# Performance work log

Measured on AMD Instinct MI355X. Metric: run time of the kernel, lower is better.

## Reference

```python
import math
import jax, jax.numpy as jnp
import numpy as np

B, S, D = 4, 2048, 512
H = 8
HD = D // H  # 64


def setup_inputs() -> dict:
    key = jax.random.key(0)
    k1, k2, k3, k4, k5 = jax.random.split(key, 5)
    x = jax.random.normal(k1, (B, S, D), dtype=jnp.float32)
    # additive causal mask, broadcast over [H, B, S, S] in the original code
    neg_inf = jnp.float32(-1e9)
    mask = jnp.where(jnp.tril(jnp.ones((S, S), dtype=bool)), 0.0, neg_inf).astype(jnp.float32)
    Wqkv = jax.random.normal(k2, (D, 3 * D), dtype=jnp.float32) * (1.0 / math.sqrt(D))
    bqkv = jax.random.normal(k3, (3 * D,), dtype=jnp.float32) * 0.02
    Wo = jax.random.normal(k4, (D, D), dtype=jnp.float32) * (1.0 / math.sqrt(D))
    bo = jax.random.normal(k5, (D,), dtype=jnp.float32) * 0.02
    return {"x": x, "mask": mask, "Wqkv": Wqkv, "bqkv": bqkv, "Wo": Wo, "bo": bo}


def reference(x, mask, Wqkv, bqkv, Wo, bo):
    b, s, d = x.shape
    hd = d // H
    qkv = x @ Wqkv + bqkv                       # [b, s, 3d]
    # match torch: reshape to [b, s, H, 3*hd], move heads, chunk last dim
    qkv = qkv.reshape(b, s, H, 3 * hd).transpose(0, 2, 1, 3)  # [b, H, s, 3hd]
    q, k, v = jnp.split(qkv, 3, axis=-1)        # each [b, H, s, hd]
    scale = 1.0 / math.sqrt(hd)
    scores = jnp.einsum('bhqd,bhkd->bhqk', q, k) * scale
    scores = scores + mask                      # mask [s, s] broadcasts over [b, H, s, s]
    attn = jax.nn.softmax(scores, axis=-1)
    vals = jnp.einsum('bhqk,bhkd->bhqd', attn, v)
    vals = vals.transpose(0, 2, 1, 3).reshape(b, s, d)
    return vals @ Wo + bo
```

## Files before the change

### kernel.cpp

```cpp
#include <hip/hip_runtime.h>
#include <hip/hip_bf16.h>

#define S_ 2048
#define D_ 512
#define HD_ 64
#define HH_ 8
#define M_ 8192

typedef __attribute__((ext_vector_type(8))) short short8;
typedef __attribute__((ext_vector_type(4))) short short4v;
typedef __attribute__((ext_vector_type(4))) float f32x4;

__device__ __forceinline__ unsigned short f2bf(float f) {
  unsigned u = __builtin_bit_cast(unsigned, f);
  u += 0x7fffu + ((u >> 16) & 1u);
  return (unsigned short)(u >> 16);
}

__device__ __forceinline__ f32x4 mfma16(short8 a, short8 b, f32x4 c) {
  return __builtin_amdgcn_mfma_f32_16x16x32_bf16(a, b, c, 0, 0, 0);
}

#define GLOAD_LDS16(gp, lp)                                                        \
  __builtin_amdgcn_global_load_lds(                                                \
      (const __attribute__((address_space(1))) void*)(gp),                         \
      (__attribute__((address_space(3))) void*)(lp), 16, 0, 0)

__global__ __launch_bounds__(256) void k_cvt_all(const float* __restrict__ x,
                                                 short* __restrict__ xb,
                                                 const float* __restrict__ wqkv,
                                                 short* __restrict__ wqkvt,
                                                 const float* __restrict__ wo,
                                                 short* __restrict__ wot) {
  __shared__ short T[32][33];
  const int bid = blockIdx.x;
  if (bid < 2048) {
    int idx = bid * 256 + threadIdx.x;
    const float4* p = (const float4*)x;
    float4 a = p[idx * 2];
    float4 b = p[idx * 2 + 1];
    short8 v;
    v[0] = (short)f2bf(a.x); v[1] = (short)f2bf(a.y);
    v[2] = (short)f2bf(a.z); v[3] = (short)f2bf(a.w);
    v[4] = (short)f2bf(b.x); v[5] = (short)f2bf(b.y);
    v[6] = (short)f2bf(b.z); v[7] = (short)f2bf(b.w);
    int row = idx >> 6;
    int dst = row * 512 + ((idx >> 3) & 7) * 64 + (((idx & 7) ^ (row & 7)) << 3);
    *(short8*)&xb[dst] = v;
    return;
  }
  const float* w;
  short* wt;
  int C, bx, by;
  if (bid < 2816) {
    w = wqkv; wt = wqkvt; C = 1536;
    int b = bid - 2048; bx = b % 48; by = b / 48;
  } else {
    w = wo; wt = wot; C = 512;
    int b = bid - 2816; bx = b % 16; by = b / 16;
  }
  const int tx = threadIdx.x & 31, ty = threadIdx.x >> 5;
  const int n0 = bx * 32, k0 = by * 32;
#pragma unroll
  for (int i = 0; i < 4; i++) {
    int k = k0 + ty + 8 * i;
    T[ty + 8 * i][tx] = (short)f2bf(w[k * C + n0 + tx]);
  }
  __syncthreads();
#pragma unroll
  for (int i = 0; i < 4; i++) {
    int n = n0 + ty + 8 * i;
    int k = k0 + tx;
    int ksw = (k & ~63) | ((((k >> 3) & 7) ^ (n & 7)) << 3) | (k & 7);
    wt[n * 512 + ksw] = T[tx][ty + 8 * i];
  }
}

template <int MODE>
__global__ __launch_bounds__(256) void k_gemm(const short* __restrict__ A,
                                              const short* __restrict__ Bt,
                                              const float* __restrict__ bias,
                                              short* __restrict__ Qo,
                                              short* __restrict__ Ko,
                                              short* __restrict__ VTo,
                                              float* __restrict__ Fo) {
  __shared__ short As[2][8192];
  __shared__ short Bs[2][4096];
  const int tid = threadIdx.x;
  const int w = tid >> 6, l = tid & 63, g = l >> 4, c = l & 15;
  const int lid = blockIdx.x;
  const int lidp = (lid & 7) * 192 + (lid >> 3);
  const int bm = (lidp / 24) * 128, bn = (lidp % 24) * 64;
  const int wm = (w >> 1) * 64, wn = (w & 1) * 32;
  f32x4 acc[4][2] = {};
  const short* Ap = A + (bm + (l >> 3)) * 512 + (l & 7) * 8;
  const short* Bp = Bt + (bn + (l >> 3)) * 512 + (l & 7) * 8;
  const int sa0 = w * 4;
  const int sb0 = w * 2;

#define GSTAGE(buf, k0)                                                       \
  {                                                                           \
    GLOAD_LDS16(Ap + (sa0 + 0) * 4096 + (k0), &As[buf][(sa0 + 0) * 512]);     \
    GLOAD_LDS16(Ap + (sa0 + 1) * 4096 + (k0), &As[buf][(sa0 + 1) * 512]);     \
    GLOAD_LDS16(Ap + (sa0 + 2) * 4096 + (k0), &As[buf][(sa0 + 2) * 512]);     \
    GLOAD_LDS16(Ap + (sa0 + 3) * 4096 + (k0), &As[buf][(sa0 + 3) * 512]);     \
    GLOAD_LDS16(Bp + (sb0 + 0) * 4096 + (k0), &Bs[buf][(sb0 + 0) * 512]);     \
    GLOAD_LDS16(Bp + (sb0 + 1) * 4096 + (k0), &Bs[buf][(sb0 + 1) * 512]);     \
  }

  GSTAGE(0, 0);
  __syncthreads();

  const int cs = c & 7;
  int cur = 0;
  for (int k0 = 0; k0 < 512; k0 += 64) {
    if (k0 + 64 < 512) GSTAGE(cur ^ 1, k0 + 64);

    short8 a0[4], a1[4], b0[2], b1[2];
#pragma unroll
    for (int mt = 0; mt < 4; mt++) {
      const short* r = &As[cur][(wm + mt * 16 + c) * 64];
      a0[mt] = *(const short8*)&r[(g ^ cs) << 3];
      a1[mt] = *(const short8*)&r[((g + 4) ^ cs) << 3];
    }
#pragma unroll
    for (int nt = 0; nt < 2; nt++) {
      const short* r = &Bs[cur][(wn + nt * 16 + c) * 64];
      b0[nt] = *(const short8*)&r[(g ^ cs) << 3];
      b1[nt] = *(const short8*)&r[((g + 4) ^ cs) << 3];
    }
#pragma unroll
    for (int mt = 0; mt < 4; mt++)
#pragma unroll
      for (int nt = 0; nt < 2; nt++) {
        acc[mt][nt] = mfma16(a0[mt], b0[nt], acc[mt][nt]);
        acc[mt][nt] = mfma16(a1[mt], b1[nt], acc[mt][nt]);
      }

    __syncthreads();
    cur ^= 1;
  }
#undef GSTAGE

  if (MODE == 0) {
    const float QS = 0.125f * 1.4426950408889634f;
#pragma unroll
    for (int nt = 0; nt < 2; nt++) {
      int n = bn + wn + nt * 16 + c;
      float bv = bias[n];
      int h = n / 192;
      int t = n - h * 192;
      int type = t >> 6;
      int hd = t & 63;
      float sc = (type == 0) ? QS : 1.0f;
#pragma unroll
      for (int mt = 0; mt < 4; mt++) {
        int m0 = bm + wm + mt * 16 + 4 * g;
        int b = m0 >> 11, ss = m0 & 2047;
        int bh = b * 8 + h;
        if (type == 2) {
          int sw = (ss & ~63) | (((((ss >> 3) & 7) ^ (hd & 7)) << 3)) | (ss & 7);
          short4v pk;
#pragma unroll
          for (int r = 0; r < 4; r++) pk[r] = (short)f2bf(acc[mt][nt][r] + bv);
          *(short4v*)&VTo[(bh * 64 + hd) * 2048 + sw] = pk;
        } else if (type == 1) {
#pragma unroll
          for (int r = 0; r < 4; r++) {
            int s = ss + r;
            int hds = ((((hd >> 3) ^ (s & 7)) << 3)) | (hd & 7);
            Ko[(bh * 2048 + s) * 64 + hds] = (short)f2bf(acc[mt][nt][r] + bv);
          }
        } else {
#pragma unroll
          for (int r = 0; r < 4; r++)
            Qo[(bh * 2048 + ss + r) * 64 + hd] = (short)f2bf((acc[mt][nt][r] + bv) * sc);
        }
      }
    }
  } else {
#pragma unroll
    for (int nt = 0; nt < 2; nt++) {
      int n = bn + wn + nt * 16 + c;
      float bv = bias[n];
#pragma unroll
      for (int mt = 0; mt < 4; mt++) {
        int m0 = bm + wm + mt * 16 + 4 * g;
#pragma unroll
        for (int r = 0; r < 4; r++) Fo[(m0 + r) * 512 + n] = acc[mt][nt][r] + bv;
      }
    }
  }
}

__global__ __launch_bounds__(256) void k_gemm2(const short* __restrict__ A,
                                               const short* __restrict__ Bt,
                                               const float* __restrict__ bias,
                                               float* __restrict__ Fo) {
  __shared__ short As[2][4096];
  __shared__ short Bs[2][4096];
  const int tid = threadIdx.x;
  const int w = tid >> 6, l = tid & 63, g = l >> 4, c = l & 15;
  const int lid = blockIdx.x;
  const int lidp = (lid & 7) * 128 + (lid >> 3);
  const int bm = (lidp >> 3) * 64, bn = (lidp & 7) * 64;
  const int wm = (w >> 1) * 32, wn = (w & 1) * 32;
  f32x4 acc[2][2] = {};
  const short* Ap = A + (bm + (l >> 3)) * 512 + (l & 7) * 8;
  const short* Bp = Bt + (bn + (l >> 3)) * 512 + (l & 7) * 8;
  const int s0 = w * 2;

#define G2STAGE(buf, k0)                                                      \
  {                                                                           \
    GLOAD_LDS16(Ap + (s0 + 0) * 4096 + (k0), &As[buf][(s0 + 0) * 512]);       \
    GLOAD_LDS16(Ap + (s0 + 1) * 4096 + (k0), &As[buf][(s0 + 1) * 512]);       \
    GLOAD_LDS16(Bp + (s0 + 0) * 4096 + (k0), &Bs[buf][(s0 + 0) * 512]);       \
    GLOAD_LDS16(Bp + (s0 + 1) * 4096 + (k0), &Bs[buf][(s0 + 1) * 512]);       \
  }

  G2STAGE(0, 0);
  __syncthreads();

  const int cs = c & 7;
  int cur = 0;
  for (int k0 = 0; k0 < 512; k0 += 64) {
    if (k0 + 64 < 512) G2STAGE(cur ^ 1, k0 + 64);

    short8 a0[2], a1[2], b0[2], b1[2];
#pragma unroll
    for (int mt = 0; mt < 2; mt++) {
      const short* r = &As[cur][(wm + mt * 16 + c) * 64];
      a0[mt] = *(const short8*)&r[(g ^ cs) << 3];
      a1[mt] = *(const short8*)&r[((g + 4) ^ cs) << 3];
    }
#pragma unroll
    for (int nt = 0; nt < 2; nt++) {
      const short* r = &Bs[cur][(wn + nt * 16 + c) * 64];
      b0[nt] = *(const short8*)&r[(g ^ cs) << 3];
      b1[nt] = *(const short8*)&r[((g + 4) ^ cs) << 3];
    }
#pragma unroll
    for (int mt = 0; mt < 2; mt++)
#pragma unroll
      for (int nt = 0; nt < 2; nt++) {
        acc[mt][nt] = mfma16(a0[mt], b0[nt], acc[mt][nt]);
        acc[mt][nt] = mfma16(a1[mt], b1[nt], acc[mt][nt]);
      }

    __syncthreads();
    cur ^= 1;
  }
#undef G2STAGE

#pragma unroll
  for (int nt = 0; nt < 2; nt++) {
    int n = bn + wn + nt * 16 + c;
    float bv = bias[n];
#pragma unroll
    for (int mt = 0; mt < 2; mt++) {
      int m0 = bm + wm + mt * 16 + 4 * g;
#pragma unroll
      for (int r = 0; r < 4; r++) Fo[(m0 + r) * 512 + n] = acc[mt][nt][r] + bv;
    }
  }
}

__global__ __launch_bounds__(512, 6) void k_attn(const short* __restrict__ Q,
                                                 const short* __restrict__ K,
                                                 const short* __restrict__ VT,
                                                 short* __restrict__ ctx) {
  __shared__ short KVs[2][8192];
  __shared__ short P[8][1024];
  const int tid = threadIdx.x;
  const int w = tid >> 6, l = tid & 63, g = l >> 4, c = l & 15;
  const int rg = w & 3, pp = w >> 2;

  const int x = blockIdx.x;
  const int bh = x & 31;
  const int j = 31 - (x >> 5);
  const int qbase = j * 64 + rg * 16;
  const int nss = j + 1;

  const short* Qb = Q + bh * S_ * HD_;
  const short* Kb = K + bh * S_ * HD_;
  const short* Vb = VT + bh * HD_ * S_;

  const int kr = tid >> 3, kc8 = (tid & 7) * 8;

#define STAGE(buf, kv0)                                                      \
  {                                                                          \
    GLOAD_LDS16(Kb + ((kv0) + kr) * 64 + kc8, &KVs[buf][w * 512]);           \
    GLOAD_LDS16(Vb + kr * 2048 + (kv0) + kc8, &KVs[buf][4096 + w * 512]);    \
  }

  short* Pw = &P[w][0];
  const int bb = bh >> 3, hh = bh & 7;
  const f32x4 CINIT = {-16.f, -16.f, -16.f, -16.f};

  short8 qf0 = *(const short8*)&Qb[(qbase + c) * 64 + 8 * g];
  short8 qf1 = *(const short8*)&Qb[(qbase + c) * 64 + 8 * g + 32];

  f32x4 o[4];
  float psum[4];
#pragma unroll
  for (int nt = 0; nt < 4; nt++) o[nt] = f32x4{0.f, 0.f, 0.f, 0.f};
#pragma unroll
  for (int r = 0; r < 4; r++) psum[r] = 0.f;

  STAGE(0, 0);
  __syncthreads();

  int cur = 0;
  for (int t = 0; t < nss; ++t) {
    if (t + 1 < nss) STAGE(cur ^ 1, (t + 1) * 64);

    const short* Kt = &KVs[cur][pp * 2048];
    const short* Vt = &KVs[cur][4096];
    const int kv0 = t * 64 + pp * 32;

    f32x4 sa[2];
#pragma unroll
    for (int nt = 0; nt < 2; nt++) {
      const short* r = &Kt[(nt * 16 + c) * 64];
      short8 kf0 = *(const short8*)&r[(g ^ (c & 7)) << 3];
      short8 kf1 = *(const short8*)&r[((g + 4) ^ (c & 7)) << 3];
      sa[nt] = mfma16(qf0, kf0, CINIT);
      sa[nt] = mfma16(qf1, kf1, sa[nt]);
    }

    if (kv0 + 32 > qbase) {
#pragma unroll
      for (int nt = 0; nt < 2; nt++) {
        int kv = kv0 + nt * 16 + c;
#pragma unroll
        for (int r = 0; r < 4; r++) {
          int qrow = qbase + 4 * g + r;
          if (kv > qrow) sa[nt][r] = -1e30f;
        }
      }
    }

#pragma unroll
    for (int nt = 0; nt < 2; nt++)
#pragma unroll
      for (int r = 0; r < 4; r++) {
        float pv = __builtin_amdgcn_exp2f(sa[nt][r]);
        psum[r] += pv;
        int row = 4 * g + r;
        int col = nt * 16 + c;
        int off = (row << 6) + ((((col >> 3) ^ (row & 7)) << 3)) + (col & 7);
        Pw[off] = (short)f2bf(pv);
      }

    short8 pa = *(const short8*)&Pw[(c << 6) + ((g ^ (c & 7)) << 3)];
#pragma unroll
    for (int nt = 0; nt < 4; nt++) {
      short8 vb = *(const short8*)&Vt[((nt * 16 + c) << 6) +
                                      (((4 * pp + g) ^ (c & 7)) << 3)];
      o[nt] = mfma16(pa, vb, o[nt]);
    }

    __syncthreads();
    cur ^= 1;
  }

#pragma unroll
  for (int off = 1; off < 16; off <<= 1)
#pragma unroll
    for (int r = 0; r < 4; r++) psum[r] += __shfl_xor(psum[r], off, 64);

  float* scr = (float*)&KVs[0][0];
  float* pscr = (float*)&P[0][0];
  if (pp == 1) {
#pragma unroll
    for (int nt = 0; nt < 4; nt++)
#pragma unroll
      for (int r = 0; r < 4; r++)
        scr[rg * 1088 + (4 * g + r) * 68 + nt * 16 + c] = o[nt][r];
    if (c == 0) {
#pragma unroll
      for (int r = 0; r < 4; r++) pscr[rg * 16 + 4 * g + r] = psum[r];
    }
  }
  __syncthreads();
  if (pp == 0) {
    float inv[4];
#pragma unroll
    for (int r = 0; r < 4; r++)
      inv[r] = 1.0f / (psum[r] + pscr[rg * 16 + 4 * g + r]);
#pragma unroll
    for (int nt = 0; nt < 4; nt++)
#pragma unroll
      for (int r = 0; r < 4; r++) {
        float ov = o[nt][r] + scr[rg * 1088 + (4 * g + r) * 68 + nt * 16 + c];
        int srow = qbase + 4 * g + r;
        int colsw = hh * 64 + (((nt * 2 + (c >> 3)) ^ (srow & 7)) << 3) + (c & 7);
        ctx[(bb * S_ + srow) * 512 + colsw] = (short)f2bf(ov * inv[r]);
      }
  }
#undef STAGE
}


extern "C" void kernel_launch(void* const* d_in, const int* in_sizes, int n_in,
                              void* d_out, int out_size, void* d_ws, size_t ws_size,
                              hipStream_t stream) {
  const float* x = (const float*)d_in[0];
  const float* Wqkv = (const float*)d_in[2];
  const float* bqkv = (const float*)d_in[3];
  const float* Wo = (const float*)d_in[4];
  const float* bo = (const float*)d_in[5];
  float* out = (float*)d_out;

  char* ws = (char*)d_ws;
  short* xb    = (short*)(ws + 0);
  short* wqkvt = (short*)(ws + 8388608);
  short* wot   = (short*)(ws + 9961472);
  short* Qw    = (short*)(ws + 10485760);
  short* Kw    = (short*)(ws + 18874368);
  short* VTw   = (short*)(ws + 27262976);
  short* ctx   = (short*)(ws + 35651584);

  k_cvt_all<<<3072, 256, 0, stream>>>(x, xb, Wqkv, wqkvt, Wo, wot);

  k_gemm<0><<<1536, 256, 0, stream>>>(xb, wqkvt, bqkv, Qw, Kw, VTw, nullptr);

  k_attn<<<1024, 512, 0, stream>>>(Qw, Kw, VTw, ctx);

  k_gemm2<<<1024, 256, 0, stream>>>(ctx, wot, bo, out);
}
```

Before: 77.65 us.

## Fuse fp32-to-bf16 conversion of x into the QKV GEMM A-tile loading

```diff
diff --git a/kernel.cpp b/kernel.cpp
--- a/kernel.cpp
+++ b/kernel.cpp
@@ -26,38 +26,21 @@
       (const __attribute__((address_space(1))) void*)(gp),                         \
       (__attribute__((address_space(3))) void*)(lp), 16, 0, 0)
 
-__global__ __launch_bounds__(256) void k_cvt_all(const float* __restrict__ x,
-                                                 short* __restrict__ xb,
-                                                 const float* __restrict__ wqkv,
-                                                 short* __restrict__ wqkvt,
-                                                 const float* __restrict__ wo,
-                                                 short* __restrict__ wot) {
+__global__ __launch_bounds__(256) void k_cvt_w(const float* __restrict__ wqkv,
+                                               short* __restrict__ wqkvt,
+                                               const float* __restrict__ wo,
+                                               short* __restrict__ wot) {
   __shared__ short T[32][33];
   const int bid = blockIdx.x;
-  if (bid < 2048) {
-    int idx = bid * 256 + threadIdx.x;
-    const float4* p = (const float4*)x;
-    float4 a = p[idx * 2];
-    float4 b = p[idx * 2 + 1];
-    short8 v;
-    v[0] = (short)f2bf(a.x); v[1] = (short)f2bf(a.y);
-    v[2] = (short)f2bf(a.z); v[3] = (short)f2bf(a.w);
-    v[4] = (short)f2bf(b.x); v[5] = (short)f2bf(b.y);
-    v[6] = (short)f2bf(b.z); v[7] = (short)f2bf(b.w);
-    int row = idx >> 6;
-    int dst = row * 512 + ((idx >> 3) & 7) * 64 + (((idx & 7) ^ (row & 7)) << 3);
-    *(short8*)&xb[dst] = v;
-    return;
-  }
   const float* w;
   short* wt;
   int C, bx, by;
-  if (bid < 2816) {
+  if (bid < 768) {
     w = wqkv; wt = wqkvt; C = 1536;
-    int b = bid - 2048; bx = b % 48; by = b / 48;
+    bx = bid % 48; by = bid / 48;
   } else {
     w = wo; wt = wot; C = 512;
-    int b = bid - 2816; bx = b % 16; by = b / 16;
+    int b = bid - 768; bx = b % 16; by = b / 16;
   }
   const int tx = threadIdx.x & 31, ty = threadIdx.x >> 5;
   const int n0 = bx * 32, k0 = by * 32;
@@ -76,14 +59,12 @@
   }
 }
 
-template <int MODE>
-__global__ __launch_bounds__(256) void k_gemm(const short* __restrict__ A,
-                                              const short* __restrict__ Bt,
-                                              const float* __restrict__ bias,
-                                              short* __restrict__ Qo,
-                                              short* __restrict__ Ko,
-                                              short* __restrict__ VTo,
-                                              float* __restrict__ Fo) {
+__global__ __launch_bounds__(256) void k_gemmx(const float* __restrict__ X,
+                                               const short* __restrict__ Bt,
+                                               const float* __restrict__ bias,
+                                               short* __restrict__ Qo,
+                                               short* __restrict__ Ko,
+                                               short* __restrict__ VTo) {
   __shared__ short As[2][8192];
   __shared__ short Bs[2][4096];
   const int tid = threadIdx.x;
@@ -93,28 +74,62 @@
   const int bm = (lidp / 24) * 128, bn = (lidp % 24) * 64;
   const int wm = (w >> 1) * 64, wn = (w & 1) * 32;
   f32x4 acc[4][2] = {};
-  const short* Ap = A + (bm + (l >> 3)) * 512 + (l & 7) * 8;
-  const short* Bp = Bt + (bn + (l >> 3)) * 512 + (l & 7) * 8;
   const int sa0 = w * 4;
   const int sb0 = w * 2;
-
-#define GSTAGE(buf, k0)                                                       \
+  const short* Bp = Bt + (bn + (l >> 3)) * 512 + (l & 7) * 8;
+
+  const float* xp[4];
+  short* lp[4][2];
+#pragma unroll
+  for (int i = 0; i < 4; i++) {
+    int s = sa0 + i;
+    int row = bm + s * 8 + (l >> 3);
+    int dc = (l & 7) ^ (row & 7);
+    xp[i] = X + row * 512 + dc * 8;
+    lp[i][0] = &As[0][s * 512 + l * 8];
+    lp[i][1] = &As[1][s * 512 + l * 8];
+  }
+
+#define BSTAGE(buf, k0)                                                       \
   {                                                                           \
-    GLOAD_LDS16(Ap + (sa0 + 0) * 4096 + (k0), &As[buf][(sa0 + 0) * 512]);     \
-    GLOAD_LDS16(Ap + (sa0 + 1) * 4096 + (k0), &As[buf][(sa0 + 1) * 512]);     \
-    GLOAD_LDS16(Ap + (sa0 + 2) * 4096 + (k0), &As[buf][(sa0 + 2) * 512]);     \
-    GLOAD_LDS16(Ap + (sa0 + 3) * 4096 + (k0), &As[buf][(sa0 + 3) * 512]);     \
     GLOAD_LDS16(Bp + (sb0 + 0) * 4096 + (k0), &Bs[buf][(sb0 + 0) * 512]);     \
     GLOAD_LDS16(Bp + (sb0 + 1) * 4096 + (k0), &Bs[buf][(sb0 + 1) * 512]);     \
   }
 
-  GSTAGE(0, 0);
+#define ALOAD(k0)                                                             \
+  {                                                                           \
+    _Pragma("unroll") for (int i = 0; i < 4; i++) {                           \
+      ua[i][0] = *(const float4*)(xp[i] + (k0));                              \
+      ua[i][1] = *(const float4*)(xp[i] + (k0) + 4);                          \
+    }                                                                         \
+  }
+
+#define AWRITE(buf)                                                           \
+  {                                                                           \
+    _Pragma("unroll") for (int i = 0; i < 4; i++) {                           \
+      short8 v;                                                               \
+      v[0] = (short)f2bf(ua[i][0].x); v[1] = (short)f2bf(ua[i][0].y);         \
+      v[2] = (short)f2bf(ua[i][0].z); v[3] = (short)f2bf(ua[i][0].w);         \
+      v[4] = (short)f2bf(ua[i][1].x); v[5] = (short)f2bf(ua[i][1].y);         \
+      v[6] = (short)f2bf(ua[i][1].z); v[7] = (short)f2bf(ua[i][1].w);         \
+      *(short8*)lp[i][buf] = v;                                               \
+    }                                                                         \
+  }
+
+  float4 ua[4][2];
+  ALOAD(0);
+  BSTAGE(0, 0);
+  AWRITE(0);
   __syncthreads();
 
   const int cs = c & 7;
   int cur = 0;
   for (int k0 = 0; k0 < 512; k0 += 64) {
-    if (k0 + 64 < 512) GSTAGE(cur ^ 1, k0 + 64);
+    const bool more = (k0 + 64 < 512);
+    if (more) {
+      ALOAD(k0 + 64);
+      BSTAGE(cur ^ 1, k0 + 64);
+    }
 
     short8 a0[4], a1[4], b0[2], b1[2];
 #pragma unroll
@@ -137,57 +152,46 @@
         acc[mt][nt] = mfma16(a1[mt], b1[nt], acc[mt][nt]);
       }
 
+    if (more) AWRITE(cur ^ 1);
     __syncthreads();
     cur ^= 1;
   }
-#undef GSTAGE
-
-  if (MODE == 0) {
-    const float QS = 0.125f * 1.4426950408889634f;
-#pragma unroll
-    for (int nt = 0; nt < 2; nt++) {
-      int n = bn + wn + nt * 16 + c;
-      float bv = bias[n];
-      int h = n / 192;
-      int t = n - h * 192;
-      int type = t >> 6;
-      int hd = t & 63;
-      float sc = (type == 0) ? QS : 1.0f;
-#pragma unroll
-      for (int mt = 0; mt < 4; mt++) {
-        int m0 = bm + wm + mt * 16 + 4 * g;
-        int b = m0 >> 11, ss = m0 & 2047;
-        int bh = b * 8 + h;
-        if (type == 2) {
-          int sw = (ss & ~63) | (((((ss >> 3) & 7) ^ (hd & 7)) << 3)) | (ss & 7);
-          short4v pk;
-#pragma unroll
-          for (int r = 0; r < 4; r++) pk[r] = (short)f2bf(acc[mt][nt][r] + bv);
-          *(short4v*)&VTo[(bh * 64 + hd) * 2048 + sw] = pk;
-        } else if (type == 1) {
-#pragma unroll
-          for (int r = 0; r < 4; r++) {
-            int s = ss + r;
-            int hds = ((((hd >> 3) ^ (s & 7)) << 3)) | (hd & 7);
-            Ko[(bh * 2048 + s) * 64 + hds] = (short)f2bf(acc[mt][nt][r] + bv);
-          }
-        } else {
-#pragma unroll
-          for (int r = 0; r < 4; r++)
-            Qo[(bh * 2048 + ss + r) * 64 + hd] = (short)f2bf((acc[mt][nt][r] + bv) * sc);
+#undef BSTAGE
+#undef ALOAD
+#undef AWRITE
+
+  const float QS = 0.125f * 1.4426950408889634f;
+#pragma unroll
+  for (int nt = 0; nt < 2; nt++) {
+    int n = bn + wn + nt * 16 + c;
+    float bv = bias[n];
+    int h = n / 192;
+    int t = n - h * 192;
+    int type = t >> 6;
+    int hd = t & 63;
+    float sc = (type == 0) ? QS : 1.0f;
+#pragma unroll
+    for (int mt = 0; mt < 4; mt++) {
+      int m0 = bm + wm + mt * 16 + 4 * g;
+      int b = m0 >> 11, ss = m0 & 2047;
+      int bh = b * 8 + h;
+      if (type == 2) {
+        int sw = (ss & ~63) | (((((ss >> 3) & 7) ^ (hd & 7)) << 3)) | (ss & 7);
+        short4v pk;
+#pragma unroll
+        for (int r = 0; r < 4; r++) pk[r] = (short)f2bf(acc[mt][nt][r] + bv);
+        *(short4v*)&VTo[(bh * 64 + hd) * 2048 + sw] = pk;
+      } else if (type == 1) {
+#pragma unroll
+        for (int r = 0; r < 4; r++) {
+          int s = ss + r;
+          int hds = ((((hd >> 3) ^ (s & 7)) << 3)) | (hd & 7);
+          Ko[(bh * 2048 + s) * 64 + hds] = (short)f2bf(acc[mt][nt][r] + bv);
         }
-      }
-    }
-  } else {
-#pragma unroll
-    for (int nt = 0; nt < 2; nt++) {
-      int n = bn + wn + nt * 16 + c;
-      float bv = bias[n];
-#pragma unroll
-      for (int mt = 0; mt < 4; mt++) {
-        int m0 = bm + wm + mt * 16 + 4 * g;
-#pragma unroll
-        for (int r = 0; r < 4; r++) Fo[(m0 + r) * 512 + n] = acc[mt][nt][r] + bv;
+      } else {
+#pragma unroll
+        for (int r = 0; r < 4; r++)
+          Qo[(bh * 2048 + ss + r) * 64 + hd] = (short)f2bf((acc[mt][nt][r] + bv) * sc);
       }
     }
   }
@@ -413,7 +417,6 @@
   float* out = (float*)d_out;
 
   char* ws = (char*)d_ws;
-  short* xb    = (short*)(ws + 0);
   short* wqkvt = (short*)(ws + 8388608);
   short* wot   = (short*)(ws + 9961472);
   short* Qw    = (short*)(ws + 10485760);
@@ -421,9 +424,9 @@
   short* VTw   = (short*)(ws + 27262976);
   short* ctx   = (short*)(ws + 35651584);
 
-  k_cvt_all<<<3072, 256, 0, stream>>>(x, xb, Wqkv, wqkvt, Wo, wot);
-
-  k_gemm<0><<<1536, 256, 0, stream>>>(xb, wqkvt, bqkv, Qw, Kw, VTw, nullptr);
+  k_cvt_w<<<1024, 256, 0, stream>>>(Wqkv, wqkvt, Wo, wot);
+
+  k_gemmx<<<1536, 256, 0, stream>>>(x, wqkvt, bqkv, Qw, Kw, VTw);
 
   k_attn<<<1024, 512, 0, stream>>>(Qw, Kw, VTw, ctx);
 
```

Measured after the change: 85.18 us. 1.1x slower.
